# Optimization experiments

Measured on AMD Instinct MI355X. Metric: run time of the kernel, lower is better.

The kernel has to match this reference:

```python
import jax, jax.numpy as jnp
import numpy as np

B, L_DEC, L_ENC = 4, 1024, 1024
D_MODEL, D_INNER, N_HEAD, D_K, D_V = 512, 256, 8, 64, 64
TEMP = D_K ** 0.5
EPS = 1e-6


def _layernorm(x, g, b):
    mu = jnp.mean(x, axis=-1, keepdims=True)
    var = jnp.mean(jnp.square(x - mu), axis=-1, keepdims=True)
    return (x - mu) * jax.lax.rsqrt(var + EPS) * g + b


def _mha(x_q, x_kv, Wq, Wk, Wv, Wfc, ln_g, ln_b, mask):
    # Faithful to source: only the query input is layer-normed; k/v use raw x_kv.
    resid = x_q
    qn = _layernorm(x_q, ln_g, ln_b)
    # Stacked per-head projections: Wq/Wk/Wv are [H, d_k, d_model]
    q = jnp.einsum('bld,hkd->bhlk', qn, Wq) / TEMP   # [B,H,Lq,dk]
    k = jnp.einsum('bld,hkd->bhlk', x_kv, Wk)        # [B,H,Lk,dk]
    v = jnp.einsum('bld,hkd->bhlk', x_kv, Wv)        # [B,H,Lk,dv]
    scores = jnp.einsum('bhqd,bhkd->bhqk', q, k)     # [B,H,Lq,Lk]
    if mask is not None:
        scores = jnp.where(mask[:, None, :, :] == 0, -jnp.inf, scores)
    attn = jax.nn.softmax(scores, axis=-1)
    out = jnp.einsum('bhqk,bhkd->bhqd', attn, v)     # [B,H,Lq,dv]
    Bq, H, Lq, dv = out.shape
    out = out.transpose(0, 2, 1, 3).reshape(Bq, Lq, H * dv)
    return out @ Wfc.T + resid


def _ffn(x, W1, b1, W2, b2, ln_g, ln_b):
    resid = x
    h = _layernorm(x, ln_g, ln_b)
    h = jax.nn.relu(h @ W1.T + b1) @ W2.T + b2
    return h + resid


def setup_inputs() -> dict:
    key = jax.random.key(0)
    ks = jax.random.split(key, 20)
    s = 0.02
    dec_input = jax.random.normal(ks[0], (B, L_DEC, D_MODEL), jnp.float32)
    enc_output = jax.random.normal(ks[1], (B, L_ENC, D_MODEL), jnp.float32)
    slf_attn_mask = jnp.tril(jnp.ones((1, L_DEC, L_DEC), jnp.int32))  # causal
    p = {}
    for i, pre in enumerate(['slf', 'enc']):
        base = 2 + i * 4
        p[f'{pre}_Wq'] = jax.random.normal(ks[base], (N_HEAD, D_K, D_MODEL), jnp.float32) * s
        p[f'{pre}_Wk'] = jax.random.normal(ks[base + 1], (N_HEAD, D_K, D_MODEL), jnp.float32) * s
        p[f'{pre}_Wv'] = jax.random.normal(ks[base + 2], (N_HEAD, D_V, D_MODEL), jnp.float32) * s
        p[f'{pre}_Wfc'] = jax.random.normal(ks[base + 3], (D_MODEL, N_HEAD * D_V), jnp.float32) * s
        p[f'{pre}_ln_g'] = jnp.ones((D_MODEL,), jnp.float32)
        p[f'{pre}_ln_b'] = jnp.zeros((D_MODEL,), jnp.float32)
    p['ffn_W1'] = jax.random.normal(ks[10], (D_INNER, D_MODEL), jnp.float32) * s
    p['ffn_b1'] = jnp.zeros((D_INNER,), jnp.float32)
    p['ffn_W2'] = jax.random.normal(ks[11], (D_MODEL, D_INNER), jnp.float32) * s
    p['ffn_b2'] = jnp.zeros((D_MODEL,), jnp.float32)
    p['ffn_ln_g'] = jnp.ones((D_MODEL,), jnp.float32)
    p['ffn_ln_b'] = jnp.zeros((D_MODEL,), jnp.float32)
    return {'dec_input': dec_input, 'enc_output': enc_output,
            'slf_attn_mask': slf_attn_mask, **p}


def reference(dec_input, enc_output,
              slf_Wq, slf_Wk, slf_Wv, slf_Wfc, slf_ln_g, slf_ln_b,
              enc_Wq, enc_Wk, enc_Wv, enc_Wfc, enc_ln_g, enc_ln_b,
              ffn_W1, ffn_b1, ffn_W2, ffn_b2, ffn_ln_g, ffn_ln_b,
              slf_attn_mask):
    x = _mha(dec_input, dec_input, slf_Wq, slf_Wk, slf_Wv, slf_Wfc,
             slf_ln_g, slf_ln_b, slf_attn_mask)
    x = _mha(x, enc_output, enc_Wq, enc_Wk, enc_Wv, enc_Wfc,
             enc_ln_g, enc_ln_b, None)
    x = _ffn(x, ffn_W1, ffn_b1, ffn_W2, ffn_b2, ffn_ln_g, ffn_ln_b)
    return x
```

## Files before the change

kernel.cpp:

```cpp
#include <hip/hip_runtime.h>
#include <hip/hip_bf16.h>
#include <math.h>

#define DMODEL 512
#define NHEAD  8
#define DHEAD  64

typedef __attribute__((ext_vector_type(8))) short bf16x8;
typedef __attribute__((ext_vector_type(4))) float f32x4;
typedef __attribute__((ext_vector_type(4))) short short4v;

static __device__ inline short f2bf(float f) {
    __hip_bfloat16 h = __float2bfloat16(f);
    return *reinterpret_cast<short*>(&h);
}

#define GLOAD_LDS16(gp, lp)                                                      \
    __builtin_amdgcn_global_load_lds(                                            \
        (const __attribute__((address_space(1))) unsigned int*)(gp),             \
        (__attribute__((address_space(3))) unsigned int*)(lp), 16, 0, 0)

struct CvtArgs {
    const float* src[12];
    short*       dst[12];
    int          n[12];
};

__global__ __launch_bounds__(256) void cvt_kernel(CvtArgs args) {
    int t = blockIdx.y;
    int idx = (blockIdx.x * 256 + threadIdx.x) * 8;
    if (idx >= args.n[t]) return;
    const float* s = args.src[t] + idx;
    float4 a = *(const float4*)s;
    float4 b = *(const float4*)(s + 4);
    bf16x8 o;
    o[0] = f2bf(a.x); o[1] = f2bf(a.y); o[2] = f2bf(a.z); o[3] = f2bf(a.w);
    o[4] = f2bf(b.x); o[5] = f2bf(b.y); o[6] = f2bf(b.z); o[7] = f2bf(b.w);
    *(bf16x8*)(args.dst[t] + idx) = o;
}

__global__ __launch_bounds__(256) void ln_kernel(const float* __restrict__ X,
                                                 const float* __restrict__ gam,
                                                 const float* __restrict__ bet,
                                                 short* __restrict__ Y) {
    int row = blockIdx.x * 4 + (threadIdx.x >> 6);
    int tid = threadIdx.x & 63;
    const float* x = X + (size_t)row * DMODEL;
    float4 a = *(const float4*)(x + tid * 4);
    float4 b = *(const float4*)(x + 256 + tid * 4);
    float sum = a.x + a.y + a.z + a.w + b.x + b.y + b.z + b.w;
    float sq  = a.x*a.x + a.y*a.y + a.z*a.z + a.w*a.w
              + b.x*b.x + b.y*b.y + b.z*b.z + b.w*b.w;
#pragma unroll
    for (int off = 1; off < 64; off <<= 1) {
        sum += __shfl_xor(sum, off);
        sq  += __shfl_xor(sq, off);
    }
    float mu  = sum * (1.0f / DMODEL);
    float var = sq * (1.0f / DMODEL) - mu * mu;
    float r   = rsqrtf(var + 1e-6f);

    float4 g1 = *(const float4*)(gam + tid * 4);
    float4 c1 = *(const float4*)(bet + tid * 4);
    float4 g2 = *(const float4*)(gam + 256 + tid * 4);
    float4 c2 = *(const float4*)(bet + 256 + tid * 4);
    short4v y1, y2;
    y1.x = f2bf((a.x - mu) * r * g1.x + c1.x);
    y1.y = f2bf((a.y - mu) * r * g1.y + c1.y);
    y1.z = f2bf((a.z - mu) * r * g1.z + c1.z);
    y1.w = f2bf((a.w - mu) * r * g1.w + c1.w);
    y2.x = f2bf((b.x - mu) * r * g2.x + c2.x);
    y2.y = f2bf((b.y - mu) * r * g2.y + c2.y);
    y2.z = f2bf((b.z - mu) * r * g2.z + c2.z);
    y2.w = f2bf((b.w - mu) * r * g2.w + c2.w);
    short* y = Y + (size_t)row * DMODEL;
    *(short4v*)(y + tid * 4)       = y1;
    *(short4v*)(y + 256 + tid * 4) = y2;
}

struct GJobs {
    const short* A[3];
    const short* W[3];
    const float* bias[3];
    const float* resid[3];
    void*        C[3];
    int M[3], N[3], K[3];
    float scale[3];
    int relu[3], obf[3], nblk[3];
};

__global__ __launch_bounds__(256) void gemm_bf16(GJobs jb) {
    __shared__ short As[64 * 64];
    __shared__ short Bs[64 * 64];

    int bid = blockIdx.x, j = 0;
    while (j < 2 && bid >= jb.nblk[j]) { bid -= jb.nblk[j]; ++j; }
    const short* __restrict__ A = jb.A[j];
    const short* __restrict__ W = jb.W[j];
    const int N = jb.N[j], K = jb.K[j];
    const int nbx = N >> 6;
    const int tn = (bid % nbx) * 64;
    const int tm = (bid / nbx) * 64;

    const int tid  = threadIdx.x;
    const int w    = tid >> 6;
    const int l    = tid & 63;
    const int lq   = l & 15;
    const int g    = l >> 4;
    const int wm   = (w >> 1) * 32;
    const int wn   = (w & 1) * 32;
    const int lrow = l >> 3;
    const int lsl  = l & 7;

    f32x4 acc[2][2];
#pragma unroll
    for (int i = 0; i < 2; ++i)
#pragma unroll
        for (int jj = 0; jj < 2; ++jj)
            acc[i][jj] = (f32x4){0.f, 0.f, 0.f, 0.f};

#pragma unroll 1
    for (int k0 = 0; k0 < K; k0 += 64) {
        __syncthreads();
#pragma unroll
        for (int i = 0; i < 2; ++i) {
            int row = i * 32 + w * 8 + lrow;
            int slot = lsl ^ (row & 7);
            GLOAD_LDS16(A + (size_t)(tm + row) * K + k0 + slot * 8,
                        As + i * 2048 + w * 512);
            GLOAD_LDS16(W + (size_t)(tn + row) * K + k0 + slot * 8,
                        Bs + i * 2048 + w * 512);
        }
        __syncthreads();

#pragma unroll
        for (int ks = 0; ks < 2; ++ks) {
            const int sl = ((ks * 4 + g) ^ (lq & 7)) * 8;
            bf16x8 af[2], bfv[2];
#pragma unroll
            for (int i = 0; i < 2; ++i) {
                af[i]  = *(const bf16x8*)&As[(wm + i * 16 + lq) * 64 + sl];
                bfv[i] = *(const bf16x8*)&Bs[(wn + i * 16 + lq) * 64 + sl];
            }
#pragma unroll
            for (int i = 0; i < 2; ++i)
#pragma unroll
                for (int jj = 0; jj < 2; ++jj)
                    acc[i][jj] = __builtin_amdgcn_mfma_f32_16x16x32_bf16(
                        af[i], bfv[jj], acc[i][jj], 0, 0, 0);
        }
    }

    const float* bias  = jb.bias[j];
    const float* resid = jb.resid[j];
    const float scale  = jb.scale[j];
    const int relu = jb.relu[j], obf = jb.obf[j];
#pragma unroll
    for (int i = 0; i < 2; ++i) {
#pragma unroll
        for (int r = 0; r < 4; ++r) {
            int row = tm + wm + i * 16 + g * 4 + r;
#pragma unroll
            for (int jj = 0; jj < 2; ++jj) {
                int col = tn + wn + jj * 16 + lq;
                float v = acc[i][jj][r] * scale;
                if (bias)  v += bias[col];
                if (resid) v += resid[(size_t)row * N + col];
                if (relu)  v = fmaxf(v, 0.f);
                if (obf) ((short*)jb.C[j])[(size_t)row * N + col] = f2bf(v);
                else     ((float*)jb.C[j])[(size_t)row * N + col] = v;
            }
        }
    }
}

__global__ __launch_bounds__(256) void attn_mfma_kernel(
        const short* __restrict__ Q, const short* __restrict__ K,
        const short* __restrict__ V, short* __restrict__ O,
        int Lq, int Lk, int causal, int qs, int kvs) {
    __shared__ short Kt[64 * 64];
    __shared__ short Vt[64][72];
    __shared__ short Pb[4][16][72];

    const int tid  = threadIdx.x;
    const int wave = tid >> 6;
    const int lane = tid & 63;
    const int lq   = lane & 15;
    const int g    = lane >> 4;
    const int bh   = blockIdx.y;
    const int b = bh >> 3, h = bh & 7;
    const int NQT = Lq >> 4;
    int gw = blockIdx.x * 4 + wave;
    const int qt = (gw & 1) ? (NQT - 1 - (gw >> 1)) : (gw >> 1);
    const int q0 = qt * 16;
    const float NEG = -__builtin_inff();

    size_t qoff = (size_t)(b * Lq + q0 + lq) * qs + h * DHEAD;
    bf16x8 qf0 = *(const bf16x8*)(Q + qoff + g * 8);
    bf16x8 qf1 = *(const bf16x8*)(Q + qoff + 32 + g * 8);

    f32x4 o[4] = {{0,0,0,0},{0,0,0,0},{0,0,0,0},{0,0,0,0}};
    f32x4 lacc = {0.f, 0.f, 0.f, 0.f};

    bf16x8 ones;
    {
        short ov = (lq == 0) ? (short)0x3F80 : (short)0;
#pragma unroll
        for (int i = 0; i < 8; ++i) ones[i] = ov;
    }

    const int nkt = causal ? ((qt >> 2) + 1) : (Lk >> 6);
    const int lrow = lane >> 3;
    const int lsl  = lane & 7;
    const int va = tid & 31;
    const int vd = (tid >> 5) * 8;

#pragma unroll 1
    for (int kt = 0; kt < nkt; ++kt) {
        __syncthreads();
#pragma unroll
        for (int i = 0; i < 2; ++i) {
            int row = i * 32 + wave * 8 + lrow;
            int slot = lsl ^ (row & 7);
            GLOAD_LDS16(K + (size_t)(b * Lk + kt * 64 + row) * kvs + h * DHEAD + slot * 8,
                        Kt + i * 2048 + wave * 512);
        }
        {
            size_t gb = (size_t)(b * Lk + kt * 64 + 2 * va) * kvs + h * DHEAD + vd;
            bf16x8 v0 = *(const bf16x8*)(V + gb);
            bf16x8 v1 = *(const bf16x8*)(V + gb + kvs);
#pragma unroll
            for (int i = 0; i < 8; ++i) {
                unsigned p = (unsigned short)v0[i] | ((unsigned)(unsigned short)v1[i] << 16);
                *(unsigned*)&Vt[vd + i][2 * va] = p;
            }
        }
        __syncthreads();

        f32x4 s[4];
#pragma unroll
        for (int sub = 0; sub < 4; ++sub) {
            int rr = sub * 16 + lq;
            const int sl0 = ((0 + g) ^ (lq & 7)) * 8;
            const int sl1 = ((4 + g) ^ (lq & 7)) * 8;
            bf16x8 kf0 = *(const bf16x8*)&Kt[rr * 64 + sl0];
            bf16x8 kf1 = *(const bf16x8*)&Kt[rr * 64 + sl1];
            f32x4 a = {0.f, 0.f, 0.f, 0.f};
            a = __builtin_amdgcn_mfma_f32_16x16x32_bf16(kf0, qf0, a, 0, 0, 0);
            a = __builtin_amdgcn_mfma_f32_16x16x32_bf16(kf1, qf1, a, 0, 0, 0);
            s[sub] = a;
        }
        if (causal && kt == nkt - 1) {
            int qg = q0 + lq;
#pragma unroll
            for (int sub = 0; sub < 4; ++sub) {
#pragma unroll
                for (int r = 0; r < 4; ++r) {
                    int kg = kt * 64 + sub * 16 + g * 4 + r;
                    if (kg > qg) s[sub][r] = NEG;
                }
            }
        }

#pragma unroll
        for (int sub = 0; sub < 4; ++sub) {
            short4v p4;
            p4.x = f2bf(__expf(fminf(s[sub][0], 60.f)));
            p4.y = f2bf(__expf(fminf(s[sub][1], 60.f)));
            p4.z = f2bf(__expf(fminf(s[sub][2], 60.f)));
            p4.w = f2bf(__expf(fminf(s[sub][3], 60.f)));
            *(short4v*)&Pb[wave][lq][sub * 16 + g * 4] = p4;
        }
        bf16x8 pf0 = *(const bf16x8*)&Pb[wave][lq][g * 8];
        bf16x8 pf1 = *(const bf16x8*)&Pb[wave][lq][32 + g * 8];

#pragma unroll
        for (int dc = 0; dc < 4; ++dc) {
            bf16x8 vf0 = *(const bf16x8*)&Vt[dc * 16 + lq][g * 8];
            bf16x8 vf1 = *(const bf16x8*)&Vt[dc * 16 + lq][32 + g * 8];
            o[dc] = __builtin_amdgcn_mfma_f32_16x16x32_bf16(pf0, vf0, o[dc], 0, 0, 0);
            o[dc] = __builtin_amdgcn_mfma_f32_16x16x32_bf16(pf1, vf1, o[dc], 0, 0, 0);
        }
        lacc = __builtin_amdgcn_mfma_f32_16x16x32_bf16(pf0, ones, lacc, 0, 0, 0);
        lacc = __builtin_amdgcn_mfma_f32_16x16x32_bf16(pf1, ones, lacc, 0, 0, 0);
    }

#pragma unroll
    for (int r = 0; r < 4; ++r) {
        float lr = __shfl(lacc[r], g << 4);
        float inv = 1.f / lr;
        size_t ob = (size_t)(b * Lq + q0 + g * 4 + r) * qs + h * DHEAD + lq;
        O[ob + 0]  = f2bf(o[0][r] * inv);
        O[ob + 16] = f2bf(o[1][r] * inv);
        O[ob + 32] = f2bf(o[2][r] * inv);
        O[ob + 48] = f2bf(o[3][r] * inv);
    }
}

static void launch_gemm(GJobs& jb, int njobs, hipStream_t stream) {
    int total = 0;
    for (int i = 0; i < 3; ++i) { if (i >= njobs) jb.nblk[i] = 0; total += jb.nblk[i]; }
    gemm_bf16<<<total, 256, 0, stream>>>(jb);
}

extern "C" void kernel_launch(void* const* d_in, const int* in_sizes, int n_in,
                              void* d_out, int out_size, void* d_ws, size_t ws_size,
                              hipStream_t stream) {
    const float* dec       = (const float*)d_in[0];
    const float* enc       = (const float*)d_in[1];
    const float* slf_Wq    = (const float*)d_in[3];
    const float* slf_Wk    = (const float*)d_in[4];
    const float* slf_Wv    = (const float*)d_in[5];
    const float* slf_Wfc   = (const float*)d_in[6];
    const float* slf_ln_g  = (const float*)d_in[7];
    const float* slf_ln_b  = (const float*)d_in[8];
    const float* enc_Wq    = (const float*)d_in[9];
    const float* enc_Wk    = (const float*)d_in[10];
    const float* enc_Wv    = (const float*)d_in[11];
    const float* enc_Wfc   = (const float*)d_in[12];
    const float* enc_ln_g  = (const float*)d_in[13];
    const float* enc_ln_b  = (const float*)d_in[14];
    const float* ffn_W1    = (const float*)d_in[15];
    const float* ffn_b1    = (const float*)d_in[16];
    const float* ffn_W2    = (const float*)d_in[17];
    const float* ffn_b2    = (const float*)d_in[18];
    const float* ffn_ln_g  = (const float*)d_in[19];
    const float* ffn_ln_b  = (const float*)d_in[20];
    float* out = (float*)d_out;

    const int Bb = 4, L = 1024, M = Bb * L;
    const size_t NE = (size_t)M * DMODEL;
    const int WQN = NHEAD * DHEAD * DMODEL;
    float* ws = (float*)d_ws;
    float* x1 = ws;
    float* x2 = ws + NE;
    short* kv16e = (short*)x2;
    short* sb = (short*)(ws + 2 * NE);
    short* dec16 = sb;               sb += NE;
    short* enc16 = sb;               sb += NE;
    short* qn16  = sb;               sb += NE;
    short* q16   = sb;               sb += NE;
    short* ao16  = sb;               sb += NE;
    short* kv16  = sb;               sb += 2 * NE;
    short* h16   = sb;               sb += NE / 2;
    short* wq_s  = sb;               sb += WQN;
    short* wkv_s = sb;               sb += 2 * WQN;
    short* wfc_s = sb;               sb += WQN;
    short* wq_e  = sb;               sb += WQN;
    short* wkv_e = sb;               sb += 2 * WQN;
    short* wfc_e = sb;               sb += WQN;
    short* w1_16 = sb;               sb += 256 * DMODEL;
    short* w2_16 = sb;               sb += DMODEL * 256;

    CvtArgs ca;
    ca.src[0] = dec;     ca.dst[0] = dec16;         ca.n[0] = (int)NE;
    ca.src[1] = enc;     ca.dst[1] = enc16;         ca.n[1] = (int)NE;
    ca.src[2] = slf_Wq;  ca.dst[2] = wq_s;          ca.n[2] = WQN;
    ca.src[3] = slf_Wk;  ca.dst[3] = wkv_s;         ca.n[3] = WQN;
    ca.src[4] = slf_Wv;  ca.dst[4] = wkv_s + WQN;   ca.n[4] = WQN;
    ca.src[5] = slf_Wfc; ca.dst[5] = wfc_s;         ca.n[5] = WQN;
    ca.src[6] = enc_Wq;  ca.dst[6] = wq_e;          ca.n[6] = WQN;
    ca.src[7] = enc_Wk;  ca.dst[7] = wkv_e;         ca.n[7] = WQN;
    ca.src[8] = enc_Wv;  ca.dst[8] = wkv_e + WQN;   ca.n[8] = WQN;
    ca.src[9] = enc_Wfc; ca.dst[9] = wfc_e;         ca.n[9] = WQN;
    ca.src[10] = ffn_W1; ca.dst[10] = w1_16;        ca.n[10] = 256 * DMODEL;
    ca.src[11] = ffn_W2; ca.dst[11] = w2_16;        ca.n[11] = DMODEL * 256;
    cvt_kernel<<<dim3(1024, 12), 256, 0, stream>>>(ca);

    dim3 attn_grid(L / 64, Bb * NHEAD);
    const int NB512  = (M / 64) * (512 / 64);
    const int NB1024 = (M / 64) * (1024 / 64);
    const int NB256  = (M / 64) * (256 / 64);

    ln_kernel<<<M / 4, 256, 0, stream>>>(dec, slf_ln_g, slf_ln_b, qn16);
    {
        GJobs jb = {};
        jb.A[0] = qn16;  jb.W[0] = wq_s;  jb.C[0] = q16;
        jb.M[0] = M; jb.N[0] = 512;  jb.K[0] = 512; jb.scale[0] = 0.125f;
        jb.obf[0] = 1; jb.nblk[0] = NB512;
        jb.A[1] = dec16; jb.W[1] = wkv_s; jb.C[1] = kv16;
        jb.M[1] = M; jb.N[1] = 1024; jb.K[1] = 512; jb.scale[1] = 1.f;
        jb.obf[1] = 1; jb.nblk[1] = NB1024;
        jb.A[2] = enc16; jb.W[2] = wkv_e; jb.C[2] = kv16e;
        jb.M[2] = M; jb.N[2] = 1024; jb.K[2] = 512; jb.scale[2] = 1.f;
        jb.obf[2] = 1; jb.nblk[2] = NB1024;
        launch_gemm(jb, 3, stream);
    }
    attn_mfma_kernel<<<attn_grid, 256, 0, stream>>>(q16, kv16, kv16 + 512, ao16,
                                                    L, L, 1, DMODEL, 1024);
    {
        GJobs jb = {};
        jb.A[0] = ao16; jb.W[0] = wfc_s; jb.resid[0] = dec; jb.C[0] = x1;
        jb.M[0] = M; jb.N[0] = 512; jb.K[0] = 512; jb.scale[0] = 1.f;
        jb.obf[0] = 0; jb.nblk[0] = NB512;
        launch_gemm(jb, 1, stream);
    }

    ln_kernel<<<M / 4, 256, 0, stream>>>(x1, enc_ln_g, enc_ln_b, qn16);
    {
        GJobs jb = {};
        jb.A[0] = qn16; jb.W[0] = wq_e; jb.C[0] = q16;
        jb.M[0] = M; jb.N[0] = 512; jb.K[0] = 512; jb.scale[0] = 0.125f;
        jb.obf[0] = 1; jb.nblk[0] = NB512;
        launch_gemm(jb, 1, stream);
    }
    attn_mfma_kernel<<<attn_grid, 256, 0, stream>>>(q16, kv16e, kv16e + 512, ao16,
                                                    L, L, 0, DMODEL, 1024);
    {
        GJobs jb = {};
        jb.A[0] = ao16; jb.W[0] = wfc_e; jb.resid[0] = x1; jb.C[0] = x2;
        jb.M[0] = M; jb.N[0] = 512; jb.K[0] = 512; jb.scale[0] = 1.f;
        jb.obf[0] = 0; jb.nblk[0] = NB512;
        launch_gemm(jb, 1, stream);
    }

    ln_kernel<<<M / 4, 256, 0, stream>>>(x2, ffn_ln_g, ffn_ln_b, qn16);
    {
        GJobs jb = {};
        jb.A[0] = qn16; jb.W[0] = w1_16; jb.bias[0] = ffn_b1; jb.C[0] = h16;
        jb.M[0] = M; jb.N[0] = 256; jb.K[0] = 512; jb.scale[0] = 1.f;
        jb.relu[0] = 1; jb.obf[0] = 1; jb.nblk[0] = NB256;
        launch_gemm(jb, 1, stream);
    }
    {
        GJobs jb = {};
        jb.A[0] = h16; jb.W[0] = w2_16; jb.bias[0] = ffn_b2; jb.resid[0] = x2;
        jb.C[0] = out;
        jb.M[0] = M; jb.N[0] = 512; jb.K[0] = 256; jb.scale[0] = 1.f;
        jb.obf[0] = 0; jb.nblk[0] = NB512;
        launch_gemm(jb, 1, stream);
    }
}
```

Baseline: 249.9 us.

## Restructure attention kernel with 32x32 MFMA, register-resident P and double-buffered K/V

The attention kernel moves from four waves of 16x16x32 MFMA tiles to two waves each handling 32 query rows with 32x32x16 MFMA. The next K/V tile is prefetched into a second LDS buffer while the current one is computed, which removes one barrier per iteration. Probabilities are rearranged between lanes with cross-half shuffles instead of a round trip through LDS. Row sums are accumulated in scalar registers rather than through an extra MFMA against a ones vector. The cost is more registers per wave and fewer waves per block, so occupancy may drop and latency hiding may suffer.

```diff
diff --git a/kernel.cpp b/kernel.cpp
--- a/kernel.cpp
+++ b/kernel.cpp
@@ -8,7 +8,9 @@
 
 typedef __attribute__((ext_vector_type(8))) short bf16x8;
 typedef __attribute__((ext_vector_type(4))) float f32x4;
+typedef __attribute__((ext_vector_type(16))) float f32x16;
 typedef __attribute__((ext_vector_type(4))) short short4v;
+typedef __attribute__((ext_vector_type(4))) unsigned int u32x4;
 
 static __device__ inline short f2bf(float f) {
     __hip_bfloat16 h = __float2bfloat16(f);
@@ -174,126 +176,163 @@
     }
 }
 
-__global__ __launch_bounds__(256) void attn_mfma_kernel(
+__global__ __launch_bounds__(128) void attn_mfma_kernel(
         const short* __restrict__ Q, const short* __restrict__ K,
         const short* __restrict__ V, short* __restrict__ O,
         int Lq, int Lk, int causal, int qs, int kvs) {
-    __shared__ short Kt[64 * 64];
-    __shared__ short Vt[64][72];
-    __shared__ short Pb[4][16][72];
+    __shared__ short Kt[2][64 * 64];
+    __shared__ short Vt[2][64 * 72];
 
     const int tid  = threadIdx.x;
     const int wave = tid >> 6;
     const int lane = tid & 63;
-    const int lq   = lane & 15;
-    const int g    = lane >> 4;
+    const int lr   = lane & 31;
+    const int h    = lane >> 5;
     const int bh   = blockIdx.y;
-    const int b = bh >> 3, h = bh & 7;
-    const int NQT = Lq >> 4;
-    int gw = blockIdx.x * 4 + wave;
-    const int qt = (gw & 1) ? (NQT - 1 - (gw >> 1)) : (gw >> 1);
-    const int q0 = qt * 16;
-    const float NEG = -__builtin_inff();
-
-    size_t qoff = (size_t)(b * Lq + q0 + lq) * qs + h * DHEAD;
-    bf16x8 qf0 = *(const bf16x8*)(Q + qoff + g * 8);
-    bf16x8 qf1 = *(const bf16x8*)(Q + qoff + 32 + g * 8);
-
-    f32x4 o[4] = {{0,0,0,0},{0,0,0,0},{0,0,0,0},{0,0,0,0}};
-    f32x4 lacc = {0.f, 0.f, 0.f, 0.f};
-
-    bf16x8 ones;
-    {
-        short ov = (lq == 0) ? (short)0x3F80 : (short)0;
-#pragma unroll
-        for (int i = 0; i < 8; ++i) ones[i] = ov;
-    }
-
-    const int nkt = causal ? ((qt >> 2) + 1) : (Lk >> 6);
-    const int lrow = lane >> 3;
-    const int lsl  = lane & 7;
-    const int va = tid & 31;
-    const int vd = (tid >> 5) * 8;
+    const int b = bh >> 3, hd = bh & 7;
+    int qx = blockIdx.x;
+    if (blockIdx.y & 16) qx = gridDim.x - 1 - qx;
+    const int q0w = qx * 64 + wave * 32;
+    const int qg  = q0w + lr;
+
+    bf16x8 qf[4];
+    {
+        size_t qoff = (size_t)(b * Lq + qg) * qs + hd * DHEAD + h * 8;
+#pragma unroll
+        for (int ks = 0; ks < 4; ++ks)
+            qf[ks] = *(const bf16x8*)(Q + qoff + ks * 16);
+    }
+
+    f32x16 o0, o1;
+#pragma unroll
+    for (int i = 0; i < 16; ++i) { o0[i] = 0.f; o1[i] = 0.f; }
+    float ltot = 0.f;
+
+    const int nkt  = causal ? (qx + 1) : (Lk >> 6);
+    const int lrow = lane >> 3, lsl = lane & 7;
+    const int va = tid & 31, vq = tid >> 5;
+    const size_t kvh = (size_t)(b * Lk) * kvs + hd * DHEAD;
+
+    {
+#pragma unroll
+        for (int i = 0; i < 4; ++i) {
+            int row = i * 16 + wave * 8 + lrow;
+            GLOAD_LDS16(K + kvh + (size_t)row * kvs + (lsl ^ lrow) * 8,
+                        &Kt[0][i * 1024 + wave * 512]);
+        }
+#pragma unroll
+        for (int d2 = 0; d2 < 2; ++d2) {
+            size_t gb = kvh + (size_t)(2 * va) * kvs + vq * 8 + d2 * 32;
+            bf16x8 v0 = *(const bf16x8*)(V + gb);
+            bf16x8 v1 = *(const bf16x8*)(V + gb + kvs);
+#pragma unroll
+            for (int i = 0; i < 8; ++i)
+                *(unsigned*)&Vt[0][(vq * 8 + d2 * 32 + i) * 72 + 2 * va] =
+                    (unsigned)(unsigned short)v0[i] |
+                    ((unsigned)(unsigned short)v1[i] << 16);
+        }
+    }
+    __syncthreads();
 
 #pragma unroll 1
     for (int kt = 0; kt < nkt; ++kt) {
+        const int cur = kt & 1, nxt = cur ^ 1;
+        const short* KT = Kt[cur];
+        const short* VT = Vt[cur];
+        const int havenext = (kt + 1 < nkt);
+        bf16x8 vn0a, vn0b, vn1a, vn1b;
+        if (havenext) {
+            const size_t kb = kvh + (size_t)((kt + 1) * 64) * kvs;
+#pragma unroll
+            for (int i = 0; i < 4; ++i) {
+                int row = i * 16 + wave * 8 + lrow;
+                GLOAD_LDS16(K + kb + (size_t)row * kvs + (lsl ^ lrow) * 8,
+                            &Kt[nxt][i * 1024 + wave * 512]);
+            }
+            size_t gb = kb + (size_t)(2 * va) * kvs + vq * 8;
+            vn0a = *(const bf16x8*)(V + gb);
+            vn0b = *(const bf16x8*)(V + gb + kvs);
+            vn1a = *(const bf16x8*)(V + gb + 32);
+            vn1b = *(const bf16x8*)(V + gb + kvs + 32);
+        }
+
+        f32x16 s0, s1;
+#pragma unroll
+        for (int i = 0; i < 16; ++i) { s0[i] = 0.f; s1[i] = 0.f; }
+#pragma unroll
+        for (int ks = 0; ks < 4; ++ks) {
+            const int sl = ((ks * 2 + h) ^ (lr & 7)) * 8;
+            bf16x8 kf0 = *(const bf16x8*)&KT[lr * 64 + sl];
+            bf16x8 kf1 = *(const bf16x8*)&KT[(32 + lr) * 64 + sl];
+            s0 = __builtin_amdgcn_mfma_f32_32x32x16_bf16(kf0, qf[ks], s0, 0, 0, 0);
+            s1 = __builtin_amdgcn_mfma_f32_32x32x16_bf16(kf1, qf[ks], s1, 0, 0, 0);
+        }
+
+        const int needmask = causal && (kt * 64 + 63 > q0w);
+        bf16x8 pa[4];
+#pragma unroll
+        for (int st = 0; st < 2; ++st) {
+            float e[16];
+#pragma unroll
+            for (int r = 0; r < 16; ++r) {
+                float sv = st ? s1[r] : s0[r];
+                if (needmask) {
+                    int kg = kt * 64 + st * 32 + (r & 3) + 8 * (r >> 2) + 4 * h;
+                    if (kg > qg) sv = -1e30f;
+                }
+                float ev = __expf(fminf(sv, 60.f));
+                e[r] = ev;
+                ltot += ev;
+            }
+            unsigned w[8], x[8];
+#pragma unroll
+            for (int i = 0; i < 8; ++i)
+                w[i] = (unsigned)(unsigned short)f2bf(e[2 * i]) |
+                       ((unsigned)(unsigned short)f2bf(e[2 * i + 1]) << 16);
+#pragma unroll
+            for (int i = 0; i < 8; ++i)
+                x[i] = (unsigned)__shfl_xor((int)w[i], 32);
+            u32x4 f0, f1;
+            f0[0] = h ? x[2] : w[0];  f0[1] = h ? x[3] : w[1];
+            f0[2] = h ? w[2] : x[0];  f0[3] = h ? w[3] : x[1];
+            f1[0] = h ? x[6] : w[4];  f1[1] = h ? x[7] : w[5];
+            f1[2] = h ? w[6] : x[4];  f1[3] = h ? w[7] : x[5];
+            pa[st * 2]     = __builtin_bit_cast(bf16x8, f0);
+            pa[st * 2 + 1] = __builtin_bit_cast(bf16x8, f1);
+        }
+
+#pragma unroll
+        for (int ks = 0; ks < 4; ++ks) {
+            const int vo = ks * 16 + h * 8;
+            bf16x8 vf0 = *(const bf16x8*)&VT[lr * 72 + vo];
+            bf16x8 vf1 = *(const bf16x8*)&VT[(32 + lr) * 72 + vo];
+            o0 = __builtin_amdgcn_mfma_f32_32x32x16_bf16(pa[ks], vf0, o0, 0, 0, 0);
+            o1 = __builtin_amdgcn_mfma_f32_32x32x16_bf16(pa[ks], vf1, o1, 0, 0, 0);
+        }
+
+        if (havenext) {
+#pragma unroll
+            for (int i = 0; i < 8; ++i) {
+                *(unsigned*)&Vt[nxt][(vq * 8 + i) * 72 + 2 * va] =
+                    (unsigned)(unsigned short)vn0a[i] |
+                    ((unsigned)(unsigned short)vn0b[i] << 16);
+                *(unsigned*)&Vt[nxt][(vq * 8 + 32 + i) * 72 + 2 * va] =
+                    (unsigned)(unsigned short)vn1a[i] |
+                    ((unsigned)(unsigned short)vn1b[i] << 16);
+            }
+        }
         __syncthreads();
-#pragma unroll
-        for (int i = 0; i < 2; ++i) {
-            int row = i * 32 + wave * 8 + lrow;
-            int slot = lsl ^ (row & 7);
-            GLOAD_LDS16(K + (size_t)(b * Lk + kt * 64 + row) * kvs + h * DHEAD + slot * 8,
-                        Kt + i * 2048 + wave * 512);
-        }
-        {
-            size_t gb = (size_t)(b * Lk + kt * 64 + 2 * va) * kvs + h * DHEAD + vd;
-            bf16x8 v0 = *(const bf16x8*)(V + gb);
-            bf16x8 v1 = *(const bf16x8*)(V + gb + kvs);
-#pragma unroll
-            for (int i = 0; i < 8; ++i) {
-                unsigned p = (unsigned short)v0[i] | ((unsigned)(unsigned short)v1[i] << 16);
-                *(unsigned*)&Vt[vd + i][2 * va] = p;
-            }
-        }
-        __syncthreads();
-
-        f32x4 s[4];
-#pragma unroll
-        for (int sub = 0; sub < 4; ++sub) {
-            int rr = sub * 16 + lq;
-            const int sl0 = ((0 + g) ^ (lq & 7)) * 8;
-            const int sl1 = ((4 + g) ^ (lq & 7)) * 8;
-            bf16x8 kf0 = *(const bf16x8*)&Kt[rr * 64 + sl0];
-            bf16x8 kf1 = *(const bf16x8*)&Kt[rr * 64 + sl1];
-            f32x4 a = {0.f, 0.f, 0.f, 0.f};
-            a = __builtin_amdgcn_mfma_f32_16x16x32_bf16(kf0, qf0, a, 0, 0, 0);
-            a = __builtin_amdgcn_mfma_f32_16x16x32_bf16(kf1, qf1, a, 0, 0, 0);
-            s[sub] = a;
-        }
-        if (causal && kt == nkt - 1) {
-            int qg = q0 + lq;
-#pragma unroll
-            for (int sub = 0; sub < 4; ++sub) {
-#pragma unroll
-                for (int r = 0; r < 4; ++r) {
-                    int kg = kt * 64 + sub * 16 + g * 4 + r;
-                    if (kg > qg) s[sub][r] = NEG;
-                }
-            }
-        }
-
-#pragma unroll
-        for (int sub = 0; sub < 4; ++sub) {
-            short4v p4;
-            p4.x = f2bf(__expf(fminf(s[sub][0], 60.f)));
-            p4.y = f2bf(__expf(fminf(s[sub][1], 60.f)));
-            p4.z = f2bf(__expf(fminf(s[sub][2], 60.f)));
-            p4.w = f2bf(__expf(fminf(s[sub][3], 60.f)));
-            *(short4v*)&Pb[wave][lq][sub * 16 + g * 4] = p4;
-        }
-        bf16x8 pf0 = *(const bf16x8*)&Pb[wave][lq][g * 8];
-        bf16x8 pf1 = *(const bf16x8*)&Pb[wave][lq][32 + g * 8];
-
-#pragma unroll
-        for (int dc = 0; dc < 4; ++dc) {
-            bf16x8 vf0 = *(const bf16x8*)&Vt[dc * 16 + lq][g * 8];
-            bf16x8 vf1 = *(const bf16x8*)&Vt[dc * 16 + lq][32 + g * 8];
-            o[dc] = __builtin_amdgcn_mfma_f32_16x16x32_bf16(pf0, vf0, o[dc], 0, 0, 0);
-            o[dc] = __builtin_amdgcn_mfma_f32_16x16x32_bf16(pf1, vf1, o[dc], 0, 0, 0);
-        }
-        lacc = __builtin_amdgcn_mfma_f32_16x16x32_bf16(pf0, ones, lacc, 0, 0, 0);
-        lacc = __builtin_amdgcn_mfma_f32_16x16x32_bf16(pf1, ones, lacc, 0, 0, 0);
-    }
-
-#pragma unroll
-    for (int r = 0; r < 4; ++r) {
-        float lr = __shfl(lacc[r], g << 4);
-        float inv = 1.f / lr;
-        size_t ob = (size_t)(b * Lq + q0 + g * 4 + r) * qs + h * DHEAD + lq;
-        O[ob + 0]  = f2bf(o[0][r] * inv);
-        O[ob + 16] = f2bf(o[1][r] * inv);
-        O[ob + 32] = f2bf(o[2][r] * inv);
-        O[ob + 48] = f2bf(o[3][r] * inv);
+    }
+
+    ltot += __shfl_xor(ltot, 32);
+    const size_t ob = (size_t)(b * Lq + q0w) * qs + hd * DHEAD + lr;
+#pragma unroll
+    for (int r = 0; r < 16; ++r) {
+        int row = (r & 3) + 8 * (r >> 2) + 4 * h;
+        float lv = __shfl(ltot, row);
+        float inv = 1.f / lv;
+        O[ob + (size_t)row * qs]      = f2bf(o0[r] * inv);
+        O[ob + (size_t)row * qs + 32] = f2bf(o1[r] * inv);
     }
 }
 
@@ -386,7 +425,7 @@
         jb.obf[2] = 1; jb.nblk[2] = NB1024;
         launch_gemm(jb, 3, stream);
     }
-    attn_mfma_kernel<<<attn_grid, 256, 0, stream>>>(q16, kv16, kv16 + 512, ao16,
+    attn_mfma_kernel<<<attn_grid, 128, 0, stream>>>(q16, kv16, kv16 + 512, ao16,
                                                     L, L, 1, DMODEL, 1024);
     {
         GJobs jb = {};
@@ -404,7 +443,7 @@
         jb.obf[0] = 1; jb.nblk[0] = NB512;
         launch_gemm(jb, 1, stream);
     }
-    attn_mfma_kernel<<<attn_grid, 256, 0, stream>>>(q16, kv16e, kv16e + 512, ao16,
+    attn_mfma_kernel<<<attn_grid, 128, 0, stream>>>(q16, kv16e, kv16e + 512, ao16,
                                                     L, L, 0, DMODEL, 1024);
     {
         GJobs jb = {};
```

Result: slower. 280.4 us (+12.2%).

## Double-buffer GEMM LDS tiles and remap blocks for XCD-local L2 reuse

Applied to the files above, without the earlier changes.

The bf16 GEMM now keeps two LDS buffers for the A and W tiles. It prefetches the next K-tile with global_load_lds while the MFMAs run on the current tile, which also removes one barrier per iteration. Block indices are also permuted so that consecutive tiles land on the same XCD, aiming to improve L2 reuse. The cost is double the LDS use, which may lower occupancy. The overlap only helps if the compiler does not force a full vmcnt wait before the LDS reads.

```diff
diff --git a/kernel.cpp b/kernel.cpp
--- a/kernel.cpp
+++ b/kernel.cpp
@@ -90,14 +90,18 @@
 };
 
 __global__ __launch_bounds__(256) void gemm_bf16(GJobs jb) {
-    __shared__ short As[64 * 64];
-    __shared__ short Bs[64 * 64];
+    __shared__ short As[2][64 * 64];
+    __shared__ short Bs[2][64 * 64];
 
     int bid = blockIdx.x, j = 0;
     while (j < 2 && bid >= jb.nblk[j]) { bid -= jb.nblk[j]; ++j; }
     const short* __restrict__ A = jb.A[j];
     const short* __restrict__ W = jb.W[j];
     const int N = jb.N[j], K = jb.K[j];
+    {
+        int nb = jb.nblk[j];
+        if ((nb & 7) == 0) bid = (bid & 7) * (nb >> 3) + (bid >> 3);
+    }
     const int nbx = N >> 6;
     const int tn = (bid % nbx) * 64;
     const int tm = (bid / nbx) * 64;
@@ -119,19 +123,34 @@
         for (int jj = 0; jj < 2; ++jj)
             acc[i][jj] = (f32x4){0.f, 0.f, 0.f, 0.f};
 
-#pragma unroll 1
-    for (int k0 = 0; k0 < K; k0 += 64) {
+    const int nkt = K >> 6;
+
+#pragma unroll
+    for (int i = 0; i < 2; ++i) {
+        int row = i * 32 + w * 8 + lrow;
+        int slot = lsl ^ (row & 7);
+        GLOAD_LDS16(A + (size_t)(tm + row) * K + slot * 8,
+                    &As[0][i * 2048 + w * 512]);
+        GLOAD_LDS16(W + (size_t)(tn + row) * K + slot * 8,
+                    &Bs[0][i * 2048 + w * 512]);
+    }
+
+#pragma unroll 2
+    for (int kt = 0; kt < nkt; ++kt) {
+        const int cur = kt & 1;
         __syncthreads();
-#pragma unroll
-        for (int i = 0; i < 2; ++i) {
-            int row = i * 32 + w * 8 + lrow;
-            int slot = lsl ^ (row & 7);
-            GLOAD_LDS16(A + (size_t)(tm + row) * K + k0 + slot * 8,
-                        As + i * 2048 + w * 512);
-            GLOAD_LDS16(W + (size_t)(tn + row) * K + k0 + slot * 8,
-                        Bs + i * 2048 + w * 512);
-        }
-        __syncthreads();
+        if (kt + 1 < nkt) {
+            const int k0n = (kt + 1) * 64;
+#pragma unroll
+            for (int i = 0; i < 2; ++i) {
+                int row = i * 32 + w * 8 + lrow;
+                int slot = lsl ^ (row & 7);
+                GLOAD_LDS16(A + (size_t)(tm + row) * K + k0n + slot * 8,
+                            &As[cur ^ 1][i * 2048 + w * 512]);
+                GLOAD_LDS16(W + (size_t)(tn + row) * K + k0n + slot * 8,
+                            &Bs[cur ^ 1][i * 2048 + w * 512]);
+            }
+        }
 
 #pragma unroll
         for (int ks = 0; ks < 2; ++ks) {
@@ -139,8 +158,8 @@
             bf16x8 af[2], bfv[2];
 #pragma unroll
             for (int i = 0; i < 2; ++i) {
-                af[i]  = *(const bf16x8*)&As[(wm + i * 16 + lq) * 64 + sl];
-                bfv[i] = *(const bf16x8*)&Bs[(wn + i * 16 + lq) * 64 + sl];
+                af[i]  = *(const bf16x8*)&As[cur][(wm + i * 16 + lq) * 64 + sl];
+                bfv[i] = *(const bf16x8*)&Bs[cur][(wn + i * 16 + lq) * 64 + sl];
             }
 #pragma unroll
             for (int i = 0; i < 2; ++i)
```

Result: faster. 243.6 us (-2.5%).
